# Kernel tuning notes

Measured on AMD Instinct MI355X. Metric: run time of the kernel, lower is better.

Reference implementation:

```python
import jax, jax.numpy as jnp
import numpy as np

B, L, D, H, DFF, K, NLVL = 8, 16384, 256, 8, 1024, 1000, 4
HD = D // H            # 32 head dim
NP = HD // 2           # 16 rotary pairs per head
GY, GX, GL = 6, 6, 4   # pairs allocated to y, x, level position dims
SPATIAL_THETA, LEVEL_THETA = 100.0, 10.0


def _freqs(n, theta):
    return theta ** (-jnp.arange(n, dtype=jnp.float32) / n)


def _layer_norm(x, g, b):
    mu = jnp.mean(x, axis=-1, keepdims=True)
    v = jnp.mean(jnp.square(x - mu), axis=-1, keepdims=True)
    return (x - mu) * jax.lax.rsqrt(v + 1e-5) * g + b


def _apply_rope(t, cos, sin):
    # t: [B, K, H, HD]; cos/sin: [B, K, 1, NP] (heads shared)
    tr = t.reshape(t.shape[:-1] + (NP, 2))
    t1, t2 = tr[..., 0], tr[..., 1]
    return jnp.stack([t1 * cos - t2 * sin, t1 * sin + t2 * cos], axis=-1).reshape(t.shape)


def setup_inputs() -> dict:
    key = jax.random.key(0)
    ks = jax.random.split(key, 12)
    N = B * L
    s = 0.02
    batch_idx = jnp.repeat(jnp.arange(B, dtype=jnp.int32), L)
    spat = jax.random.randint(ks[3], (2, N), 0, 32, dtype=jnp.int32)
    lvl = jax.random.randint(ks[4], (1, N), 0, NLVL, dtype=jnp.int32)
    return {
        "queries": jax.random.normal(ks[0], (N, D), jnp.float32),
        "query_batch_offsets": jnp.arange(B + 1, dtype=jnp.int32) * L,
        "token_predicted_salience_score": jax.random.uniform(ks[1], (N,), jnp.float32),
        "token_electron_scores": jax.random.uniform(ks[2], (N,), jnp.float32),
        "query_spatial_indices": jnp.concatenate([batch_idx[None], spat, lvl], axis=0),
        "stacked_feature_maps": jnp.zeros((1,), jnp.float32),  # unused (neighborhood attn off)
        "level_spatial_shapes": jnp.array([[256, 256], [128, 128], [64, 64], [32, 32]], jnp.int32),
        "Wqkv": jax.random.normal(ks[5], (D, 3 * D), jnp.float32) * s,
        "Wo": jax.random.normal(ks[6], (D, D), jnp.float32) * s,
        "ln1_g": jnp.ones((D,), jnp.float32), "ln1_b": jnp.zeros((D,), jnp.float32),
        "W1": jax.random.normal(ks[7], (D, DFF), jnp.float32) * s,
        "b1": jnp.zeros((DFF,), jnp.float32),
        "W2": jax.random.normal(ks[8], (DFF, D), jnp.float32) * s,
        "b2": jnp.zeros((D,), jnp.float32),
        "ln2_g": jnp.ones((D,), jnp.float32), "ln2_b": jnp.zeros((D,), jnp.float32),
    }


def reference(queries, query_batch_offsets, token_predicted_salience_score,
              query_spatial_indices, stacked_feature_maps, level_spatial_shapes,
              token_electron_scores, Wqkv, Wo, ln1_g, ln1_b, W1, b1, W2, b2, ln2_g, ln2_b):
    # --- per-batch top-k salience selection (equal-length fast path) ---
    scores = (token_electron_scores + token_predicted_salience_score).reshape(B, L)
    _, idx = jax.lax.top_k(jax.lax.stop_gradient(scores), K)           # [B, K]
    topk_indices = (idx + query_batch_offsets[:-1, None]).reshape(-1)  # [B*K]

    # --- gather selected tokens ---
    x = queries[topk_indices]                          # [B*K, D]
    sp = query_spatial_indices[:, topk_indices]        # [4, B*K]
    pos = sp[1:3].T.astype(jnp.float32)                # [B*K, 2] (y, x)
    lvl = sp[3]
    shapes_f = level_spatial_shapes.astype(jnp.float32)
    pos = pos * (shapes_f[0][None, :] / shapes_f[lvl])  # rescale to finest level
    lvl_f = lvl.astype(jnp.float32)

    ang = jnp.concatenate([
        pos[:, 0:1] * _freqs(GY, SPATIAL_THETA)[None, :],
        pos[:, 1:2] * _freqs(GX, SPATIAL_THETA)[None, :],
        lvl_f[:, None] * _freqs(GL, LEVEL_THETA)[None, :],
    ], axis=-1)                                        # [B*K, NP]
    cos = jnp.cos(ang).reshape(B, K, 1, NP)
    sin = jnp.sin(ang).reshape(B, K, 1, NP)

    # --- pre-norm RoPE self-attention over selected tokens ---
    h = _layer_norm(x, ln1_g, ln1_b)
    qkv = h @ Wqkv                                     # [B*K, 3D]
    q, k, v = [t.reshape(B, K, H, HD) for t in jnp.split(qkv, 3, axis=-1)]
    q = _apply_rope(q, cos, sin)
    k = _apply_rope(k, cos, sin)
    att = jnp.einsum('bqhd,bkhd->bhqk', q, k) / jnp.sqrt(jnp.float32(HD))
    att = jax.nn.softmax(att, axis=-1)
    out = jnp.einsum('bhqk,bkhd->bqhd', att, v).reshape(B * K, D) @ Wo
    sa_out = x + out

    # --- scatter (index_copy) back ---
    queries = queries.at[topk_indices].set(sa_out)

    # --- pre-norm FFN on all tokens ---
    h2 = _layer_norm(queries, ln2_g, ln2_b)
    queries = queries + (jax.nn.gelu(h2 @ W1 + b1) @ W2 + b2)
    return queries
```

## Files before the change

### kernel.cpp

```cpp
#include <hip/hip_runtime.h>
#include <hip/hip_bf16.h>
#include <math.h>

#define B_   8
#define L_   16384
#define D_   256
#define H_   8
#define DFF_ 1024
#define KSEL 1000
#define NTOK (B_*KSEL)
#define NALL (B_*L_)
#define HD_  32
#define NP_  16

typedef float f32x4 __attribute__((ext_vector_type(4)));
typedef short s16x8 __attribute__((ext_vector_type(8)));
typedef unsigned short u16x8 __attribute__((ext_vector_type(8)));
typedef unsigned short u16x4 __attribute__((ext_vector_type(4)));

static __device__ __forceinline__ unsigned short f2bf(float f) {
  __bf16 b = (__bf16)f;
  return __builtin_bit_cast(unsigned short, b);
}
static __device__ __forceinline__ float bf2f(unsigned short h) {
  return __uint_as_float(((unsigned)h) << 16);
}
static __device__ __forceinline__ f32x4 mfma_bf16(s16x8 a, s16x8 b, f32x4 c) {
  return __builtin_amdgcn_mfma_f32_16x16x32_bf16(a, b, c, 0, 0, 0);
}

__global__ __launch_bounds__(256) void transpose_all(
    const float* Wqkv, const float* Wo, const float* W1, const float* W2,
    unsigned short* Wqkvt, unsigned short* Wot, unsigned short* W1t, unsigned short* W2t) {
  __shared__ float tile[32][33];
  int bid = blockIdx.x;
  const float* src; unsigned short* dst; int K, N, tl;
  if (bid < 192)      { src = Wqkv; dst = Wqkvt; K = 256;  N = 768;  tl = bid; }
  else if (bid < 256) { src = Wo;   dst = Wot;   K = 256;  N = 256;  tl = bid - 192; }
  else if (bid < 512) { src = W1;   dst = W1t;   K = 256;  N = 1024; tl = bid - 256; }
  else                { src = W2;   dst = W2t;   K = 1024; N = 256;  tl = bid - 512; }
  int ntx = N >> 5;
  int n0 = (tl % ntx) * 32, k0 = (tl / ntx) * 32;
  int tx = threadIdx.x & 31, ty = threadIdx.x >> 5;
#pragma unroll
  for (int r = 0; r < 32; r += 8)
    tile[ty + r][tx] = src[(size_t)(k0 + ty + r) * N + n0 + tx];
  __syncthreads();
#pragma unroll
  for (int r = 0; r < 32; r += 8)
    dst[(size_t)(n0 + ty + r) * K + k0 + tx] = f2bf(tile[tx][ty + r]);
}

__global__ __launch_bounds__(1024) void topk_kernel(const float* es, const float* ss, int* out_idx) {
  __shared__ int wsum[16];
  __shared__ int chunk_base;
  int b = blockIdx.x;
  int t = threadIdx.x;
  int lane = t & 63, w = t >> 6;
  int base = b * L_;
  unsigned kreg[16];
#pragma unroll
  for (int ci = 0; ci < 16; ++ci) {
    int i = ci * 1024 + t;
    float f = es[base + i] + ss[base + i];
    unsigned u = __float_as_uint(f);
    kreg[ci] = (u & 0x80000000u) ? ~u : (u | 0x80000000u);
  }
  unsigned v = 0;
  for (int bit = 31; bit >= 0; --bit) {
    unsigned cand = v | (1u << bit);
    int c = 0;
#pragma unroll
    for (int ci = 0; ci < 16; ++ci) c += (kreg[ci] >= cand) ? 1 : 0;
    for (int m = 1; m < 64; m <<= 1) c += __shfl_xor(c, m);
    if (lane == 0) wsum[w] = c;
    __syncthreads();
    int tot = 0;
#pragma unroll
    for (int j = 0; j < 16; ++j) tot += wsum[j];
    if (tot >= KSEL) v = cand;
    __syncthreads();
  }
  if (t == 0) chunk_base = 0;
  __syncthreads();
  for (int pass = 0; pass < 2; ++pass) {
    for (int ci = 0; ci < 16; ++ci) {
      bool pred = (pass == 0) ? (kreg[ci] > v) : (kreg[ci] == v);
      unsigned long long mask = __ballot(pred);
      if (lane == 0) wsum[w] = __popcll(mask);
      __syncthreads();
      int wbase = chunk_base;
      for (int j = 0; j < w; ++j) wbase += wsum[j];
      if (pred) {
        int pos = wbase + __popcll(mask & ((1ull << lane) - 1ull));
        if (pos < KSEL) out_idx[b * KSEL + pos] = base + ci * 1024 + t;
      }
      __syncthreads();
      if (t == 0) { int tt = 0; for (int j = 0; j < 16; ++j) tt += wsum[j]; chunk_base += tt; }
      __syncthreads();
    }
  }
}

__global__ __launch_bounds__(256) void gather_ln_rope(
    const float* queries, const int* idx, const int* spat, const int* shapes,
    const float* g1, const float* b1ln, unsigned short* h, float* cosb, float* sinb) {
  int tok = blockIdx.x;
  int t = threadIdx.x;
  int gidx = idx[tok];
  float x = queries[(size_t)gidx * D_ + t];
  float s1 = x, s2 = x * x;
  for (int m = 1; m < 64; m <<= 1) { s1 += __shfl_xor(s1, m); s2 += __shfl_xor(s2, m); }
  __shared__ float p1[4], p2[4];
  int w = t >> 6;
  if ((t & 63) == 0) { p1[w] = s1; p2[w] = s2; }
  __syncthreads();
  float tot  = p1[0] + p1[1] + p1[2] + p1[3];
  float tot2 = p2[0] + p2[1] + p2[2] + p2[3];
  float mu = tot / D_;
  float var = tot2 / D_ - mu * mu;
  float rs = 1.0f / sqrtf(var + 1e-5f);
  h[(size_t)tok * D_ + t] = f2bf((x - mu) * rs * g1[t] + b1ln[t]);
  if (t < NP_) {
    int yy = spat[1*(size_t)NALL + gidx];
    int xx = spat[2*(size_t)NALL + gidx];
    int lv = spat[3*(size_t)NALL + gidx];
    float ang;
    if (t < 6) {
      float sc = (float)shapes[0] / (float)shapes[lv*2+0];
      ang = (float)yy * sc * powf(100.0f, -(float)t / 6.0f);
    } else if (t < 12) {
      float sc = (float)shapes[1] / (float)shapes[lv*2+1];
      ang = (float)xx * sc * powf(100.0f, -(float)(t-6) / 6.0f);
    } else {
      ang = (float)lv * powf(10.0f, -(float)(t-12) / 4.0f);
    }
    cosb[tok*NP_ + t] = cosf(ang);
    sinb[tok*NP_ + t] = sinf(ang);
  }
}

__global__ __launch_bounds__(256) void qkv_gemm(
    const unsigned short* h, const unsigned short* Wt,
    unsigned short* qh, unsigned short* kh, unsigned short* vh) {
  __shared__ unsigned short a_lds[64][264];
  int m0 = blockIdx.y * 64;
  int n0 = blockIdx.x * 128;
  int t = threadIdx.x, lane = t & 63, w = t >> 6;
  int lm = lane & 15, lg = lane >> 4;
  for (int it = 0; it < 8; ++it) {
    int c = it*256 + t;
    int row = c >> 5, off = (c & 31) * 8;
    *(uint4*)&a_lds[row][off] = *(const uint4*)&h[(size_t)(m0+row)*D_ + off];
  }
  __syncthreads();
  f32x4 acc[8];
#pragma unroll
  for (int i = 0; i < 8; ++i) acc[i] = (f32x4){0.f,0.f,0.f,0.f};
#pragma unroll
  for (int ks = 0; ks < 8; ++ks) {
    s16x8 a = *(const s16x8*)&a_lds[w*16 + lm][ks*32 + lg*8];
#pragma unroll
    for (int nt = 0; nt < 8; ++nt) {
      s16x8 bb = *(const s16x8*)&Wt[(size_t)(n0 + nt*16 + lm)*D_ + ks*32 + lg*8];
      acc[nt] = mfma_bf16(a, bb, acc[nt]);
    }
  }
#pragma unroll
  for (int i = 0; i < 4; ++i) {
    int row = w*16 + lg*4 + i;
    int tok = m0 + row;
    int b = tok / 1000, tk = tok - b*1000;
#pragma unroll
    for (int nt = 0; nt < 8; ++nt) {
      int col = n0 + nt*16 + lm;
      int part = col >> 8;
      int within = col & 255;
      int head = within >> 5, d = within & 31;
      unsigned short* dst = part == 0 ? qh : (part == 1 ? kh : vh);
      dst[(size_t)((b*H_ + head)*1000 + tk)*HD_ + d] = f2bf(acc[nt][i]);
    }
  }
}

__global__ __launch_bounds__(256) void attn_kernel(
    const unsigned short* qh, const unsigned short* kh, const unsigned short* vh,
    const float* cosb, const float* sinb, unsigned short* obuf) {
  __shared__ unsigned short k_lds[64][40];
  __shared__ unsigned short vt_lds[32][72];
  __shared__ unsigned short p_lds[4][16][72];
  int bh = blockIdx.y;
  int b = bh >> 3, hh = bh & 7;
  int q0 = blockIdx.x * 64;
  int t = threadIdx.x, lane = t & 63, w = t >> 6;
  int lm = lane & 15, lg = lane >> 4;

  int qrow = q0 + w*16 + lm;
  int qtk = qrow < 999 ? qrow : 999;
  int qtokg = b*1000 + qtk;
  s16x8 qf;
  {
    u16x8 raw = *(const u16x8*)&qh[(size_t)(bh*1000 + qtk)*HD_ + lg*8];
    f32x4 c4 = *(const f32x4*)&cosb[(size_t)qtokg*NP_ + lg*4];
    f32x4 s4 = *(const f32x4*)&sinb[(size_t)qtokg*NP_ + lg*4];
#pragma unroll
    for (int m = 0; m < 4; ++m) {
      float t1 = bf2f(raw[2*m]), t2 = bf2f(raw[2*m+1]);
      float e = t1*c4[m] - t2*s4[m];
      float o = t1*s4[m] + t2*c4[m];
      qf[2*m]   = (short)f2bf(e);
      qf[2*m+1] = (short)f2bf(o);
    }
  }

  float m_run[4], l_run[4];
  f32x4 o_acc[2];
#pragma unroll
  for (int i = 0; i < 4; ++i) { m_run[i] = -1e30f; l_run[i] = 0.f; }
  o_acc[0] = (f32x4){0.f,0.f,0.f,0.f};
  o_acc[1] = (f32x4){0.f,0.f,0.f,0.f};

  for (int ch = 0; ch < 16; ++ch) {
    int c0 = ch * 64;
    __syncthreads();
    for (int it = 0; it < 4; ++it) {
      int pi = it*256 + t;
      int key = pi >> 4, pp = pi & 15;
      int tk = c0 + key; tk = tk < 999 ? tk : 999;
      int tokg = b*1000 + tk;
      unsigned raw = *(const unsigned*)&kh[(size_t)(bh*1000 + tk)*HD_ + pp*2];
      float cc = cosb[(size_t)tokg*NP_ + pp], scn = sinb[(size_t)tokg*NP_ + pp];
      float t1 = bf2f((unsigned short)(raw & 0xFFFFu));
      float t2 = bf2f((unsigned short)(raw >> 16));
      float e = t1*cc - t2*scn, od = t1*scn + t2*cc;
      unsigned outp = (unsigned)f2bf(e) | ((unsigned)f2bf(od) << 16);
      *(unsigned*)&k_lds[key][pp*2] = outp;
    }
    for (int it = 0; it < 4; ++it) {
      int e2 = it*256 + t;
      int key = e2 >> 4, dp = e2 & 15;
      int tk = c0 + key; tk = tk < 999 ? tk : 999;
      unsigned raw = *(const unsigned*)&vh[(size_t)(bh*1000 + tk)*HD_ + dp*2];
      vt_lds[dp*2][key]   = (unsigned short)(raw & 0xFFFFu);
      vt_lds[dp*2+1][key] = (unsigned short)(raw >> 16);
    }
    __syncthreads();
    f32x4 sacc[4];
#pragma unroll
    for (int nt = 0; nt < 4; ++nt) {
      sacc[nt] = (f32x4){0.f,0.f,0.f,0.f};
      s16x8 bb = *(const s16x8*)&k_lds[nt*16 + lm][lg*8];
      sacc[nt] = mfma_bf16(qf, bb, sacc[nt]);
    }
    const float scale = 0.17677669529663687f;
#pragma unroll
    for (int nt = 0; nt < 4; ++nt) {
      int col = c0 + nt*16 + lm;
      bool valid = col < 1000;
#pragma unroll
      for (int i = 0; i < 4; ++i) sacc[nt][i] = valid ? sacc[nt][i]*scale : -1e30f;
    }
#pragma unroll
    for (int i = 0; i < 4; ++i) {
      float mx = fmaxf(fmaxf(sacc[0][i], sacc[1][i]), fmaxf(sacc[2][i], sacc[3][i]));
      for (int m = 1; m < 16; m <<= 1) mx = fmaxf(mx, __shfl_xor(mx, m));
      float mn = fmaxf(m_run[i], mx);
      float alpha = __expf(m_run[i] - mn);
      float rsum = 0.f;
#pragma unroll
      for (int nt = 0; nt < 4; ++nt) { float p = __expf(sacc[nt][i] - mn); sacc[nt][i] = p; rsum += p; }
      for (int m = 1; m < 16; m <<= 1) rsum += __shfl_xor(rsum, m);
      l_run[i] = l_run[i]*alpha + rsum;
      m_run[i] = mn;
      o_acc[0][i] *= alpha; o_acc[1][i] *= alpha;
    }
#pragma unroll
    for (int nt = 0; nt < 4; ++nt)
#pragma unroll
      for (int i = 0; i < 4; ++i)
        p_lds[w][lg*4 + i][nt*16 + lm] = f2bf(sacc[nt][i]);
#pragma unroll
    for (int kk = 0; kk < 2; ++kk) {
      s16x8 pf = *(const s16x8*)&p_lds[w][lm][kk*32 + lg*8];
#pragma unroll
      for (int dt = 0; dt < 2; ++dt) {
        s16x8 vf = *(const s16x8*)&vt_lds[dt*16 + lm][kk*32 + lg*8];
        o_acc[dt] = mfma_bf16(pf, vf, o_acc[dt]);
      }
    }
  }
#pragma unroll
  for (int i = 0; i < 4; ++i) {
    int qr = q0 + w*16 + lg*4 + i;
    if (qr < 1000) {
      float innorm = 1.0f / l_run[i];
      int tokg = b*1000 + qr;
#pragma unroll
      for (int dt = 0; dt < 2; ++dt)
        obuf[(size_t)tokg*D_ + hh*HD_ + dt*16 + lm] = f2bf(o_acc[dt][i] * innorm);
    }
  }
}

__global__ __launch_bounds__(256) void wo_scatter(
    const unsigned short* obuf, const unsigned short* Wot,
    const float* queries, const int* idx, float* sa, int* slot_of) {
  __shared__ unsigned short a_lds[64][264];
  int m0 = blockIdx.x * 64;
  int t = threadIdx.x, lane = t & 63, w = t >> 6;
  int lm = lane & 15, lg = lane >> 4;
  for (int it = 0; it < 8; ++it) {
    int c = it*256 + t;
    int row = c >> 5, off = (c & 31) * 8;
    *(uint4*)&a_lds[row][off] = *(const uint4*)&obuf[(size_t)(m0+row)*D_ + off];
  }
  if (t < 64) { int tok = m0 + t; slot_of[idx[tok]] = tok; }
  __syncthreads();
  f32x4 acc[16];
#pragma unroll
  for (int i = 0; i < 16; ++i) acc[i] = (f32x4){0.f,0.f,0.f,0.f};
#pragma unroll
  for (int ks = 0; ks < 8; ++ks) {
    s16x8 a = *(const s16x8*)&a_lds[w*16 + lm][ks*32 + lg*8];
#pragma unroll
    for (int nt = 0; nt < 16; ++nt) {
      s16x8 bb = *(const s16x8*)&Wot[(size_t)(nt*16 + lm)*D_ + ks*32 + lg*8];
      acc[nt] = mfma_bf16(a, bb, acc[nt]);
    }
  }
#pragma unroll
  for (int i = 0; i < 4; ++i) {
    int row = w*16 + lg*4 + i;
    int tok = m0 + row;
    int g = idx[tok];
#pragma unroll
    for (int nt = 0; nt < 16; ++nt) {
      int col = nt*16 + lm;
      sa[(size_t)tok*D_ + col] = queries[(size_t)g*D_ + col] + acc[nt][i];
    }
  }
}

__global__ __launch_bounds__(512, 4) void ffn_kernel(
    const float* queries, const float* sa, const int* slot_of,
    const unsigned short* W1t, const unsigned short* W2t,
    const float* b1, const float* b2, const float* g2, const float* bb2,
    float* out) {
  __shared__ unsigned short h2_lds[64][264];
  __shared__ unsigned short c1_lds[64][136];
  int m0 = blockIdx.x * 64;
  int t = threadIdx.x, lane = t & 63, w = t >> 6;
  int lm = lane & 15, lg = lane >> 4;
  f32x4 g2v  = *(const f32x4*)&g2[lane*4];
  f32x4 bb2v = *(const f32x4*)&bb2[lane*4];
#pragma unroll
  for (int rr = 0; rr < 8; ++rr) {
    int row = w*8 + rr;
    int grow = m0 + row;
    int slot = slot_of[grow];
    const float* xb = (slot >= 0) ? (sa + (size_t)slot * D_) : (queries + (size_t)grow * D_);
    f32x4 x = *(const f32x4*)&xb[lane*4];
    float s1 = x[0]+x[1]+x[2]+x[3];
    float s2 = x[0]*x[0]+x[1]*x[1]+x[2]*x[2]+x[3]*x[3];
    for (int m = 1; m < 64; m <<= 1) { s1 += __shfl_xor(s1, m); s2 += __shfl_xor(s2, m); }
    float mu = s1 * (1.0f/D_);
    float rs = __builtin_amdgcn_rsqf(s2 * (1.0f/D_) - mu*mu + 1e-5f);
    u16x4 hv;
#pragma unroll
    for (int j = 0; j < 4; ++j) hv[j] = f2bf((x[j]-mu)*rs*g2v[j] + bb2v[j]);
    *(u16x4*)&h2_lds[row][lane*4] = hv;
  }
  __syncthreads();
  f32x4 acc2[4][2];
#pragma unroll
  for (int mi = 0; mi < 4; ++mi) { acc2[mi][0] = (f32x4){0.f,0.f,0.f,0.f}; acc2[mi][1] = (f32x4){0.f,0.f,0.f,0.f}; }

  const unsigned short* w1p = W1t + (size_t)(w*16 + lm) * D_ + lg*8;
  const unsigned short* w2p = W2t + (size_t)(w*32 + lm) * DFF_ + lg*8;

  for (int chn = 0; chn < 8; ++chn) {
    int d0 = chn * 128;
    s16x8 b1f[8];
#pragma unroll
    for (int ks = 0; ks < 8; ++ks)
      b1f[ks] = *(const s16x8*)(w1p + (size_t)d0 * D_ + ks*32);
    f32x4 acc1[4];
#pragma unroll
    for (int mi = 0; mi < 4; ++mi) acc1[mi] = (f32x4){0.f,0.f,0.f,0.f};
#pragma unroll
    for (int ks = 0; ks < 8; ++ks)
#pragma unroll
      for (int mi = 0; mi < 4; ++mi) {
        s16x8 a = *(const s16x8*)&h2_lds[mi*16 + lm][ks*32 + lg*8];
        acc1[mi] = mfma_bf16(a, b1f[ks], acc1[mi]);
      }
    s16x8 b2f[2][4];
#pragma unroll
    for (int nj = 0; nj < 2; ++nj)
#pragma unroll
      for (int ks = 0; ks < 4; ++ks)
        b2f[nj][ks] = *(const s16x8*)(w2p + (size_t)nj*16*DFF_ + d0 + ks*32);
    float bias = b1[d0 + w*16 + lm];
#pragma unroll
    for (int mi = 0; mi < 4; ++mi)
#pragma unroll
      for (int i = 0; i < 4; ++i) {
        float xv = acc1[mi][i] + bias;
        float z = 0.7978845608028654f * xv * fmaf(xv*xv, 0.044715f, 1.0f);
        float e = __builtin_amdgcn_exp2f(z * -2.885390081777927f);
        float r = __builtin_amdgcn_rcpf(1.0f + e);
        float th = fmaf(-2.0f*e, r, 1.0f);
        float y = 0.5f * xv;
        y = fmaf(y, th, y);
        c1_lds[mi*16 + lg*4 + i][w*16 + lm] = f2bf(y);
      }
    __syncthreads();
#pragma unroll
    for (int ks = 0; ks < 4; ++ks) {
      s16x8 a[4];
#pragma unroll
      for (int mi = 0; mi < 4; ++mi) a[mi] = *(const s16x8*)&c1_lds[mi*16 + lm][ks*32 + lg*8];
#pragma unroll
      for (int nj = 0; nj < 2; ++nj)
#pragma unroll
        for (int mi = 0; mi < 4; ++mi) acc2[mi][nj] = mfma_bf16(a[mi], b2f[nj][ks], acc2[mi][nj]);
    }
    __syncthreads();
  }
  float b2v0 = b2[w*32 + lm], b2v1 = b2[w*32 + 16 + lm];
#pragma unroll
  for (int mi = 0; mi < 4; ++mi)
#pragma unroll
    for (int i = 0; i < 4; ++i) {
      int grow = m0 + mi*16 + lg*4 + i;
      int slot = slot_of[grow];
      const float* xb = (slot >= 0) ? (sa + (size_t)slot * D_) : (queries + (size_t)grow * D_);
      size_t rbase = (size_t)grow * D_;
      int c0 = w*32 + lm;
      out[rbase + c0]      = xb[c0]      + acc2[mi][0][i] + b2v0;
      out[rbase + c0 + 16] = xb[c0 + 16] + acc2[mi][1][i] + b2v1;
    }
}

extern "C" void kernel_launch(void* const* d_in, const int* in_sizes, int n_in,
                              void* d_out, int out_size, void* d_ws, size_t ws_size,
                              hipStream_t stream) {
  const float* queries = (const float*)d_in[0];
  const float* sal   = (const float*)d_in[2];
  const float* ele   = (const float*)d_in[3];
  const int*   spat  = (const int*)d_in[4];
  const int*   shapes= (const int*)d_in[6];
  const float* Wqkv  = (const float*)d_in[7];
  const float* Wo    = (const float*)d_in[8];
  const float* ln1g  = (const float*)d_in[9];
  const float* ln1b  = (const float*)d_in[10];
  const float* W1    = (const float*)d_in[11];
  const float* b1    = (const float*)d_in[12];
  const float* W2    = (const float*)d_in[13];
  const float* b2    = (const float*)d_in[14];
  const float* ln2g  = (const float*)d_in[15];
  const float* ln2b  = (const float*)d_in[16];
  float* out = (float*)d_out;

  char* ws = (char*)d_ws;
  size_t off = 0;
  auto alloc = [&](size_t bytes) -> void* {
    void* p = ws + off;
    off = (off + bytes + 255) & ~(size_t)255;
    return p;
  };
  int*            idxb  = (int*)alloc((size_t)NTOK * 4);
  unsigned short* h     = (unsigned short*)alloc((size_t)NTOK * D_ * 2);
  float*          cosb  = (float*)alloc((size_t)NTOK * NP_ * 4);
  float*          sinb  = (float*)alloc((size_t)NTOK * NP_ * 4);
  unsigned short* qh    = (unsigned short*)alloc((size_t)NTOK * D_ * 2);
  unsigned short* kh    = (unsigned short*)alloc((size_t)NTOK * D_ * 2);
  unsigned short* vh    = (unsigned short*)alloc((size_t)NTOK * D_ * 2);
  unsigned short* obuf  = (unsigned short*)alloc((size_t)NTOK * D_ * 2);
  unsigned short* Wqkvt = (unsigned short*)alloc((size_t)768 * 256 * 2);
  unsigned short* Wot   = (unsigned short*)alloc((size_t)256 * 256 * 2);
  unsigned short* W1t   = (unsigned short*)alloc((size_t)1024 * 256 * 2);
  unsigned short* W2t   = (unsigned short*)alloc((size_t)256 * 1024 * 2);
  float*          sa    = (float*)alloc((size_t)NTOK * D_ * 4);
  int*            slot  = (int*)alloc((size_t)NALL * 4);

  hipMemsetAsync(slot, 0xFF, (size_t)NALL * 4, stream);
  transpose_all<<<768, 256, 0, stream>>>(Wqkv, Wo, W1, W2, Wqkvt, Wot, W1t, W2t);
  topk_kernel<<<B_, 1024, 0, stream>>>(ele, sal, idxb);
  gather_ln_rope<<<NTOK, 256, 0, stream>>>(queries, idxb, spat, shapes, ln1g, ln1b, h, cosb, sinb);
  qkv_gemm<<<dim3(6, 125), 256, 0, stream>>>(h, Wqkvt, qh, kh, vh);
  attn_kernel<<<dim3(16, 64), 256, 0, stream>>>(qh, kh, vh, cosb, sinb, obuf);
  wo_scatter<<<125, 256, 0, stream>>>(obuf, Wot, queries, idxb, sa, slot);
  ffn_kernel<<<2048, 512, 0, stream>>>(queries, sa, slot, W1t, W2t, b1, b2, ln2g, ln2b, out);
}
```

Before: 485.8 us.

## Restructure FFN kernel with 32x32 MFMA, 1024-thread blocks and split-K reduction

```diff
diff --git a/kernel.cpp b/kernel.cpp
--- a/kernel.cpp
+++ b/kernel.cpp
@@ -14,6 +14,7 @@
 #define NP_  16
 
 typedef float f32x4 __attribute__((ext_vector_type(4)));
+typedef float f32x16 __attribute__((ext_vector_type(16)));
 typedef short s16x8 __attribute__((ext_vector_type(8)));
 typedef unsigned short u16x8 __attribute__((ext_vector_type(8)));
 typedef unsigned short u16x4 __attribute__((ext_vector_type(4)));
@@ -27,6 +28,12 @@
 }
 static __device__ __forceinline__ f32x4 mfma_bf16(s16x8 a, s16x8 b, f32x4 c) {
   return __builtin_amdgcn_mfma_f32_16x16x32_bf16(a, b, c, 0, 0, 0);
+}
+static __device__ __forceinline__ f32x16 mfma32(s16x8 a, s16x8 b, f32x16 c) {
+  return __builtin_amdgcn_mfma_f32_32x32x16_bf16(a, b, c, 0, 0, 0);
+}
+static __device__ __forceinline__ int swz(int cshort, int row) {
+  return cshort ^ (((row >> 3) & 3) << 3);
 }
 
 __global__ __launch_bounds__(256) void transpose_all(
@@ -341,105 +348,129 @@
   }
 }
 
-__global__ __launch_bounds__(512, 4) void ffn_kernel(
+__global__ __launch_bounds__(1024, 4) void ffn_kernel(
     const float* queries, const float* sa, const int* slot_of,
     const unsigned short* W1t, const unsigned short* W2t,
     const float* b1, const float* b2, const float* g2, const float* bb2,
     float* out) {
-  __shared__ unsigned short h2_lds[64][264];
-  __shared__ unsigned short c1_lds[64][136];
+  __shared__ unsigned short h2[64][264];
+  __shared__ unsigned short c1[64][520];
   int m0 = blockIdx.x * 64;
   int t = threadIdx.x, lane = t & 63, w = t >> 6;
-  int lm = lane & 15, lg = lane >> 4;
-  f32x4 g2v  = *(const f32x4*)&g2[lane*4];
-  f32x4 bb2v = *(const f32x4*)&bb2[lane*4];
-#pragma unroll
-  for (int rr = 0; rr < 8; ++rr) {
-    int row = w*8 + rr;
-    int grow = m0 + row;
-    int slot = slot_of[grow];
-    const float* xb = (slot >= 0) ? (sa + (size_t)slot * D_) : (queries + (size_t)grow * D_);
-    f32x4 x = *(const f32x4*)&xb[lane*4];
-    float s1 = x[0]+x[1]+x[2]+x[3];
-    float s2 = x[0]*x[0]+x[1]*x[1]+x[2]*x[2]+x[3]*x[3];
-    for (int m = 1; m < 64; m <<= 1) { s1 += __shfl_xor(s1, m); s2 += __shfl_xor(s2, m); }
-    float mu = s1 * (1.0f/D_);
-    float rs = __builtin_amdgcn_rsqf(s2 * (1.0f/D_) - mu*mu + 1e-5f);
-    u16x4 hv;
-#pragma unroll
-    for (int j = 0; j < 4; ++j) hv[j] = f2bf((x[j]-mu)*rs*g2v[j] + bb2v[j]);
-    *(u16x4*)&h2_lds[row][lane*4] = hv;
-  }
-  __syncthreads();
-  f32x4 acc2[4][2];
-#pragma unroll
-  for (int mi = 0; mi < 4; ++mi) { acc2[mi][0] = (f32x4){0.f,0.f,0.f,0.f}; acc2[mi][1] = (f32x4){0.f,0.f,0.f,0.f}; }
-
-  const unsigned short* w1p = W1t + (size_t)(w*16 + lm) * D_ + lg*8;
-  const unsigned short* w2p = W2t + (size_t)(w*32 + lm) * DFF_ + lg*8;
-
-  for (int chn = 0; chn < 8; ++chn) {
-    int d0 = chn * 128;
-    s16x8 b1f[8];
-#pragma unroll
-    for (int ks = 0; ks < 8; ++ks)
-      b1f[ks] = *(const s16x8*)(w1p + (size_t)d0 * D_ + ks*32);
-    f32x4 acc1[4];
-#pragma unroll
-    for (int mi = 0; mi < 4; ++mi) acc1[mi] = (f32x4){0.f,0.f,0.f,0.f};
-#pragma unroll
-    for (int ks = 0; ks < 8; ++ks)
-#pragma unroll
-      for (int mi = 0; mi < 4; ++mi) {
-        s16x8 a = *(const s16x8*)&h2_lds[mi*16 + lm][ks*32 + lg*8];
-        acc1[mi] = mfma_bf16(a, b1f[ks], acc1[mi]);
-      }
-    s16x8 b2f[2][4];
-#pragma unroll
-    for (int nj = 0; nj < 2; ++nj)
-#pragma unroll
-      for (int ks = 0; ks < 4; ++ks)
-        b2f[nj][ks] = *(const s16x8*)(w2p + (size_t)nj*16*DFF_ + d0 + ks*32);
-    float bias = b1[d0 + w*16 + lm];
-#pragma unroll
-    for (int mi = 0; mi < 4; ++mi)
-#pragma unroll
-      for (int i = 0; i < 4; ++i) {
-        float xv = acc1[mi][i] + bias;
-        float z = 0.7978845608028654f * xv * fmaf(xv*xv, 0.044715f, 1.0f);
-        float e = __builtin_amdgcn_exp2f(z * -2.885390081777927f);
-        float r = __builtin_amdgcn_rcpf(1.0f + e);
-        float th = fmaf(-2.0f*e, r, 1.0f);
-        float y = 0.5f * xv;
-        y = fmaf(y, th, y);
-        c1_lds[mi*16 + lg*4 + i][w*16 + lm] = f2bf(y);
-      }
-    __syncthreads();
-#pragma unroll
-    for (int ks = 0; ks < 4; ++ks) {
-      s16x8 a[4];
-#pragma unroll
-      for (int mi = 0; mi < 4; ++mi) a[mi] = *(const s16x8*)&c1_lds[mi*16 + lm][ks*32 + lg*8];
-#pragma unroll
-      for (int nj = 0; nj < 2; ++nj)
-#pragma unroll
-        for (int mi = 0; mi < 4; ++mi) acc2[mi][nj] = mfma_bf16(a[mi], b2f[nj][ks], acc2[mi][nj]);
-    }
-    __syncthreads();
-  }
-  float b2v0 = b2[w*32 + lm], b2v1 = b2[w*32 + 16 + lm];
-#pragma unroll
-  for (int mi = 0; mi < 4; ++mi)
-#pragma unroll
-    for (int i = 0; i < 4; ++i) {
-      int grow = m0 + mi*16 + lg*4 + i;
+  int l31 = lane & 31;
+  int koff = (lane >> 5) * 8;
+  {
+    f32x4 g2v  = *(const f32x4*)&g2[(lane & 63) * 4];
+    f32x4 bb2v = *(const f32x4*)&bb2[(lane & 63) * 4];
+#pragma unroll
+    for (int rr = 0; rr < 4; ++rr) {
+      int row = w*4 + rr;
+      int grow = m0 + row;
       int slot = slot_of[grow];
       const float* xb = (slot >= 0) ? (sa + (size_t)slot * D_) : (queries + (size_t)grow * D_);
-      size_t rbase = (size_t)grow * D_;
-      int c0 = w*32 + lm;
-      out[rbase + c0]      = xb[c0]      + acc2[mi][0][i] + b2v0;
-      out[rbase + c0 + 16] = xb[c0 + 16] + acc2[mi][1][i] + b2v1;
-    }
+      f32x4 x = *(const f32x4*)&xb[lane*4];
+      float s1 = x[0]+x[1]+x[2]+x[3];
+      float s2 = x[0]*x[0]+x[1]*x[1]+x[2]*x[2]+x[3]*x[3];
+      for (int m = 1; m < 64; m <<= 1) { s1 += __shfl_xor(s1, m); s2 += __shfl_xor(s2, m); }
+      float mu = s1 * (1.0f/D_);
+      float rs = __builtin_amdgcn_rsqf(s2 * (1.0f/D_) - mu*mu + 1e-5f);
+      u16x4 hv;
+#pragma unroll
+      for (int j = 0; j < 4; ++j) hv[j] = f2bf((x[j]-mu)*rs*g2v[j] + bb2v[j]);
+      *(u16x4*)&h2[row][swz(lane*4, row)] = hv;
+    }
+  }
+  __syncthreads();
+
+  f32x16 acc2_0 = {}, acc2_1 = {};
+  int kh = w >> 3;
+  int cg = w & 7;
+  const unsigned short* w2p = W2t + (size_t)(cg*32 + l31) * DFF_ + kh*256 + koff;
+
+  for (int chn = 0; chn < 2; ++chn) {
+    int d0 = chn * 512;
+    f32x16 acc1_0 = {}, acc1_1 = {};
+    const unsigned short* w1p = W1t + (size_t)(d0 + w*32 + l31) * D_ + koff;
+#pragma unroll
+    for (int kb = 0; kb < 4; ++kb) {
+      s16x8 bg0 = *(const s16x8*)(w1p + (kb*4+0)*16);
+      s16x8 bg1 = *(const s16x8*)(w1p + (kb*4+1)*16);
+      s16x8 bg2 = *(const s16x8*)(w1p + (kb*4+2)*16);
+      s16x8 bg3 = *(const s16x8*)(w1p + (kb*4+3)*16);
+#pragma unroll
+      for (int j = 0; j < 4; ++j) {
+        int c = (kb*4 + j) * 16 + koff;
+        s16x8 a0 = *(const s16x8*)&h2[l31][swz(c, l31)];
+        s16x8 a1 = *(const s16x8*)&h2[l31 + 32][swz(c, l31)];
+        s16x8 bj = j == 0 ? bg0 : j == 1 ? bg1 : j == 2 ? bg2 : bg3;
+        acc1_0 = mfma32(a0, bj, acc1_0);
+        acc1_1 = mfma32(a1, bj, acc1_1);
+      }
+    }
+    {
+      int col = w*32 + l31;
+      float bias = b1[d0 + col];
+#pragma unroll
+      for (int tile = 0; tile < 2; ++tile)
+#pragma unroll
+        for (int r = 0; r < 16; ++r) {
+          float xv = (tile == 0 ? acc1_0[r] : acc1_1[r]) + bias;
+          float z = 0.7978845608028654f * xv * fmaf(xv*xv, 0.044715f, 1.0f);
+          float e = __builtin_amdgcn_exp2f(z * -2.885390081777927f);
+          float rcp = __builtin_amdgcn_rcpf(1.0f + e);
+          float th = fmaf(-2.0f*e, rcp, 1.0f);
+          float y = 0.5f * xv;
+          y = fmaf(y, th, y);
+          int row = tile*32 + (r&3) + 8*(r>>2) + 4*(lane>>5);
+          c1[row][swz(col, row)] = f2bf(y);
+        }
+    }
+    __syncthreads();
+#pragma unroll
+    for (int kb = 0; kb < 4; ++kb) {
+      s16x8 bg0 = *(const s16x8*)(w2p + d0 + (kb*4+0)*16);
+      s16x8 bg1 = *(const s16x8*)(w2p + d0 + (kb*4+1)*16);
+      s16x8 bg2 = *(const s16x8*)(w2p + d0 + (kb*4+2)*16);
+      s16x8 bg3 = *(const s16x8*)(w2p + d0 + (kb*4+3)*16);
+#pragma unroll
+      for (int j = 0; j < 4; ++j) {
+        int c = kh*256 + (kb*4 + j) * 16 + koff;
+        s16x8 a0 = *(const s16x8*)&c1[l31][swz(c, l31)];
+        s16x8 a1 = *(const s16x8*)&c1[l31 + 32][swz(c, l31)];
+        s16x8 bj = j == 0 ? bg0 : j == 1 ? bg1 : j == 2 ? bg2 : bg3;
+        acc2_0 = mfma32(a0, bj, acc2_0);
+        acc2_1 = mfma32(a1, bj, acc2_1);
+      }
+    }
+    __syncthreads();
+  }
+  float* red = (float*)&c1[0][0];
+  if (kh == 1) {
+    int col = cg*32 + l31;
+#pragma unroll
+    for (int tile = 0; tile < 2; ++tile)
+#pragma unroll
+      for (int r = 0; r < 16; ++r) {
+        int row = tile*32 + (r&3) + 8*(r>>2) + 4*(lane>>5);
+        red[row*257 + col] = (tile == 0 ? acc2_0[r] : acc2_1[r]);
+      }
+  }
+  __syncthreads();
+  if (kh == 0) {
+    int col = cg*32 + l31;
+    float bias = b2[col];
+#pragma unroll
+    for (int tile = 0; tile < 2; ++tile)
+#pragma unroll
+      for (int r = 0; r < 16; ++r) {
+        int row = tile*32 + (r&3) + 8*(r>>2) + 4*(lane>>5);
+        int grow = m0 + row;
+        int slot = slot_of[grow];
+        const float* xb = (slot >= 0) ? (sa + (size_t)slot * D_) : (queries + (size_t)grow * D_);
+        float v = (tile == 0 ? acc2_0[r] : acc2_1[r]) + red[row*257 + col] + xb[col] + bias;
+        out[(size_t)grow * D_ + col] = v;
+      }
+  }
 }
 
 extern "C" void kernel_launch(void* const* d_in, const int* in_sizes, int n_in,
@@ -491,5 +522,5 @@
   qkv_gemm<<<dim3(6, 125), 256, 0, stream>>>(h, Wqkvt, qh, kh, vh);
   attn_kernel<<<dim3(16, 64), 256, 0, stream>>>(qh, kh, vh, cosb, sinb, obuf);
   wo_scatter<<<125, 256, 0, stream>>>(obuf, Wot, queries, idxb, sa, slot);
-  ffn_kernel<<<2048, 512, 0, stream>>>(queries, sa, slot, W1t, W2t, b1, b2, ln2g, ln2b, out);
-}
+  ffn_kernel<<<2048, 1024, 0, stream>>>(queries, sa, slot, W1t, W2t, b1, b2, ln2g, ln2b, out);
+}
```

Result: slower. 579.0 us (+19.2%).

## Restructure FFN kernel: swap MFMA operands, wider DFF chunks, vectorized epilogue

Applied to the files above, without the earlier changes.

```diff
diff --git a/kernel.cpp b/kernel.cpp
--- a/kernel.cpp
+++ b/kernel.cpp
@@ -346,100 +346,123 @@
     const unsigned short* W1t, const unsigned short* W2t,
     const float* b1, const float* b2, const float* g2, const float* bb2,
     float* out) {
-  __shared__ unsigned short h2_lds[64][264];
-  __shared__ unsigned short c1_lds[64][136];
+  __shared__ unsigned short h2[64][264];
+  __shared__ unsigned short c1[64][264];
   int m0 = blockIdx.x * 64;
   int t = threadIdx.x, lane = t & 63, w = t >> 6;
   int lm = lane & 15, lg = lane >> 4;
-  f32x4 g2v  = *(const f32x4*)&g2[lane*4];
-  f32x4 bb2v = *(const f32x4*)&bb2[lane*4];
-#pragma unroll
-  for (int rr = 0; rr < 8; ++rr) {
-    int row = w*8 + rr;
-    int grow = m0 + row;
+  {
+    f32x4 g2v  = *(const f32x4*)&g2[lane*4];
+    f32x4 bb2v = *(const f32x4*)&bb2[lane*4];
+#pragma unroll
+    for (int rr = 0; rr < 8; ++rr) {
+      int row = w*8 + rr;
+      int grow = m0 + row;
+      int slot = slot_of[grow];
+      const float* xb = (slot >= 0) ? (sa + (size_t)slot * D_) : (queries + (size_t)grow * D_);
+      f32x4 x = *(const f32x4*)&xb[lane*4];
+      float s1 = x[0]+x[1]+x[2]+x[3];
+      float s2 = x[0]*x[0]+x[1]*x[1]+x[2]*x[2]+x[3]*x[3];
+      for (int m = 1; m < 64; m <<= 1) { s1 += __shfl_xor(s1, m); s2 += __shfl_xor(s2, m); }
+      float mu = s1 * (1.0f/D_);
+      float rs = __builtin_amdgcn_rsqf(s2 * (1.0f/D_) - mu*mu + 1e-5f);
+      u16x4 hv;
+#pragma unroll
+      for (int j = 0; j < 4; ++j) hv[j] = f2bf((x[j]-mu)*rs*g2v[j] + bb2v[j]);
+      *(u16x4*)&h2[row][lane*4] = hv;
+    }
+  }
+  __syncthreads();
+
+  f32x4 acc2[2][4];
+#pragma unroll
+  for (int at = 0; at < 2; ++at)
+#pragma unroll
+    for (int rt = 0; rt < 4; ++rt) acc2[at][rt] = (f32x4){0.f,0.f,0.f,0.f};
+
+  const unsigned short* w2p = W2t + (size_t)(w*32 + lm) * DFF_ + lg*8;
+
+  for (int chn = 0; chn < 4; ++chn) {
+    int d0 = chn * 256;
+    f32x4 acc1[2][4];
+#pragma unroll
+    for (int at = 0; at < 2; ++at)
+#pragma unroll
+      for (int rt = 0; rt < 4; ++rt) acc1[at][rt] = (f32x4){0.f,0.f,0.f,0.f};
+    const unsigned short* w1p = W1t + (size_t)(d0 + w*32 + lm) * D_ + lg*8;
+#pragma unroll
+    for (int ks = 0; ks < 8; ++ks) {
+      s16x8 wa0 = *(const s16x8*)(w1p + ks*32);
+      s16x8 wa1 = *(const s16x8*)(w1p + 16*D_ + ks*32);
+      s16x8 f0 = *(const s16x8*)&h2[lm     ][ks*32 + lg*8];
+      s16x8 f1 = *(const s16x8*)&h2[lm + 16][ks*32 + lg*8];
+      s16x8 f2 = *(const s16x8*)&h2[lm + 32][ks*32 + lg*8];
+      s16x8 f3 = *(const s16x8*)&h2[lm + 48][ks*32 + lg*8];
+      acc1[0][0] = mfma_bf16(wa0, f0, acc1[0][0]);
+      acc1[0][1] = mfma_bf16(wa0, f1, acc1[0][1]);
+      acc1[0][2] = mfma_bf16(wa0, f2, acc1[0][2]);
+      acc1[0][3] = mfma_bf16(wa0, f3, acc1[0][3]);
+      acc1[1][0] = mfma_bf16(wa1, f0, acc1[1][0]);
+      acc1[1][1] = mfma_bf16(wa1, f1, acc1[1][1]);
+      acc1[1][2] = mfma_bf16(wa1, f2, acc1[1][2]);
+      acc1[1][3] = mfma_bf16(wa1, f3, acc1[1][3]);
+    }
+#pragma unroll
+    for (int at = 0; at < 2; ++at) {
+      f32x4 b1v = *(const f32x4*)&b1[d0 + w*32 + at*16 + lg*4];
+#pragma unroll
+      for (int rt = 0; rt < 4; ++rt) {
+        u16x4 pv;
+#pragma unroll
+        for (int i = 0; i < 4; ++i) {
+          float xv = acc1[at][rt][i] + b1v[i];
+          float z = 0.7978845608028654f * xv * fmaf(xv*xv, 0.044715f, 1.0f);
+          float e = __builtin_amdgcn_exp2f(z * -2.885390081777927f);
+          float rcp = __builtin_amdgcn_rcpf(1.0f + e);
+          float th = fmaf(-2.0f*e, rcp, 1.0f);
+          float y = 0.5f * xv;
+          y = fmaf(y, th, y);
+          pv[i] = f2bf(y);
+        }
+        *(u16x4*)&c1[rt*16 + lm][w*32 + at*16 + lg*4] = pv;
+      }
+    }
+    __syncthreads();
+#pragma unroll
+    for (int ks = 0; ks < 8; ++ks) {
+      s16x8 wa0 = *(const s16x8*)(w2p + d0 + ks*32);
+      s16x8 wa1 = *(const s16x8*)(w2p + (size_t)16*DFF_ + d0 + ks*32);
+      s16x8 f0 = *(const s16x8*)&c1[lm     ][ks*32 + lg*8];
+      s16x8 f1 = *(const s16x8*)&c1[lm + 16][ks*32 + lg*8];
+      s16x8 f2 = *(const s16x8*)&c1[lm + 32][ks*32 + lg*8];
+      s16x8 f3 = *(const s16x8*)&c1[lm + 48][ks*32 + lg*8];
+      acc2[0][0] = mfma_bf16(wa0, f0, acc2[0][0]);
+      acc2[0][1] = mfma_bf16(wa0, f1, acc2[0][1]);
+      acc2[0][2] = mfma_bf16(wa0, f2, acc2[0][2]);
+      acc2[0][3] = mfma_bf16(wa0, f3, acc2[0][3]);
+      acc2[1][0] = mfma_bf16(wa1, f0, acc2[1][0]);
+      acc2[1][1] = mfma_bf16(wa1, f1, acc2[1][1]);
+      acc2[1][2] = mfma_bf16(wa1, f2, acc2[1][2]);
+      acc2[1][3] = mfma_bf16(wa1, f3, acc2[1][3]);
+    }
+    __syncthreads();
+  }
+#pragma unroll
+  for (int rt = 0; rt < 4; ++rt) {
+    int grow = m0 + rt*16 + lm;
     int slot = slot_of[grow];
     const float* xb = (slot >= 0) ? (sa + (size_t)slot * D_) : (queries + (size_t)grow * D_);
-    f32x4 x = *(const f32x4*)&xb[lane*4];
-    float s1 = x[0]+x[1]+x[2]+x[3];
-    float s2 = x[0]*x[0]+x[1]*x[1]+x[2]*x[2]+x[3]*x[3];
-    for (int m = 1; m < 64; m <<= 1) { s1 += __shfl_xor(s1, m); s2 += __shfl_xor(s2, m); }
-    float mu = s1 * (1.0f/D_);
-    float rs = __builtin_amdgcn_rsqf(s2 * (1.0f/D_) - mu*mu + 1e-5f);
-    u16x4 hv;
-#pragma unroll
-    for (int j = 0; j < 4; ++j) hv[j] = f2bf((x[j]-mu)*rs*g2v[j] + bb2v[j]);
-    *(u16x4*)&h2_lds[row][lane*4] = hv;
-  }
-  __syncthreads();
-  f32x4 acc2[4][2];
-#pragma unroll
-  for (int mi = 0; mi < 4; ++mi) { acc2[mi][0] = (f32x4){0.f,0.f,0.f,0.f}; acc2[mi][1] = (f32x4){0.f,0.f,0.f,0.f}; }
-
-  const unsigned short* w1p = W1t + (size_t)(w*16 + lm) * D_ + lg*8;
-  const unsigned short* w2p = W2t + (size_t)(w*32 + lm) * DFF_ + lg*8;
-
-  for (int chn = 0; chn < 8; ++chn) {
-    int d0 = chn * 128;
-    s16x8 b1f[8];
-#pragma unroll
-    for (int ks = 0; ks < 8; ++ks)
-      b1f[ks] = *(const s16x8*)(w1p + (size_t)d0 * D_ + ks*32);
-    f32x4 acc1[4];
-#pragma unroll
-    for (int mi = 0; mi < 4; ++mi) acc1[mi] = (f32x4){0.f,0.f,0.f,0.f};
-#pragma unroll
-    for (int ks = 0; ks < 8; ++ks)
-#pragma unroll
-      for (int mi = 0; mi < 4; ++mi) {
-        s16x8 a = *(const s16x8*)&h2_lds[mi*16 + lm][ks*32 + lg*8];
-        acc1[mi] = mfma_bf16(a, b1f[ks], acc1[mi]);
-      }
-    s16x8 b2f[2][4];
-#pragma unroll
-    for (int nj = 0; nj < 2; ++nj)
-#pragma unroll
-      for (int ks = 0; ks < 4; ++ks)
-        b2f[nj][ks] = *(const s16x8*)(w2p + (size_t)nj*16*DFF_ + d0 + ks*32);
-    float bias = b1[d0 + w*16 + lm];
-#pragma unroll
-    for (int mi = 0; mi < 4; ++mi)
-#pragma unroll
-      for (int i = 0; i < 4; ++i) {
-        float xv = acc1[mi][i] + bias;
-        float z = 0.7978845608028654f * xv * fmaf(xv*xv, 0.044715f, 1.0f);
-        float e = __builtin_amdgcn_exp2f(z * -2.885390081777927f);
-        float r = __builtin_amdgcn_rcpf(1.0f + e);
-        float th = fmaf(-2.0f*e, r, 1.0f);
-        float y = 0.5f * xv;
-        y = fmaf(y, th, y);
-        c1_lds[mi*16 + lg*4 + i][w*16 + lm] = f2bf(y);
-      }
-    __syncthreads();
-#pragma unroll
-    for (int ks = 0; ks < 4; ++ks) {
-      s16x8 a[4];
-#pragma unroll
-      for (int mi = 0; mi < 4; ++mi) a[mi] = *(const s16x8*)&c1_lds[mi*16 + lm][ks*32 + lg*8];
-#pragma unroll
-      for (int nj = 0; nj < 2; ++nj)
-#pragma unroll
-        for (int mi = 0; mi < 4; ++mi) acc2[mi][nj] = mfma_bf16(a[mi], b2f[nj][ks], acc2[mi][nj]);
-    }
-    __syncthreads();
-  }
-  float b2v0 = b2[w*32 + lm], b2v1 = b2[w*32 + 16 + lm];
-#pragma unroll
-  for (int mi = 0; mi < 4; ++mi)
-#pragma unroll
-    for (int i = 0; i < 4; ++i) {
-      int grow = m0 + mi*16 + lg*4 + i;
-      int slot = slot_of[grow];
-      const float* xb = (slot >= 0) ? (sa + (size_t)slot * D_) : (queries + (size_t)grow * D_);
-      size_t rbase = (size_t)grow * D_;
-      int c0 = w*32 + lm;
-      out[rbase + c0]      = xb[c0]      + acc2[mi][0][i] + b2v0;
-      out[rbase + c0 + 16] = xb[c0 + 16] + acc2[mi][1][i] + b2v1;
-    }
+#pragma unroll
+    for (int at = 0; at < 2; ++at) {
+      int oc = w*32 + at*16 + lg*4;
+      f32x4 b2v = *(const f32x4*)&b2[oc];
+      f32x4 xv = *(const f32x4*)&xb[oc];
+      f32x4 v;
+#pragma unroll
+      for (int i = 0; i < 4; ++i) v[i] = acc2[at][rt][i] + xv[i] + b2v[i];
+      *(f32x4*)&out[(size_t)grow * D_ + oc] = v;
+    }
+  }
 }
 
 extern "C" void kernel_launch(void* const* d_in, const int* in_sizes, int n_in,
```

New measurement: 495.4 us. No clear change (+2.0%).
